# Performance work log

Measured on AMD Instinct MI355X. Metric: run time of the kernel, lower is better.

The kernel has to match this reference:

```python
import jax, jax.numpy as jnp
import numpy as np

NH = 8      # num_heads
AG = 49     # agent_num
PS = 7      # pool_size = sqrt(agent_num)


def _pool_mat(in_size, out_size):
    # torch AdaptiveAvgPool2d bin boundaries: start=floor(i*n/o), end=ceil((i+1)*n/o)
    P = np.zeros((out_size, in_size), dtype=np.float32)
    for i in range(out_size):
        s = (i * in_size) // out_size
        e = -((-(i + 1) * in_size) // out_size)
        P[i, s:e] = 1.0 / (e - s)
    return jnp.asarray(P)


def setup_inputs() -> dict:
    key = jax.random.key(0)
    ks = jax.random.split(key, 16)
    b, n, dim, ic, cc = 32, 1024, 512, 512, 256
    s = 0.02
    d = {}
    d['x'] = jax.random.normal(ks[0], (b, n, dim), jnp.float32)
    d['context'] = jax.random.normal(ks[1], (b, n, cc), jnp.float32)
    d['Wq'] = jax.random.normal(ks[2], (dim, ic), jnp.float32) * s
    d['Wkv'] = jax.random.normal(ks[3], (dim, 2 * ic), jnp.float32) * s
    d['conv_w'] = jax.random.normal(ks[4], (ic, ic + cc, 3, 3), jnp.float32) * s
    d['conv_b'] = jnp.zeros((ic,), jnp.float32)
    d['dwc_w'] = jax.random.normal(ks[5], (ic, 1, 3, 3), jnp.float32) * s
    d['dwc_b'] = jnp.zeros((ic,), jnp.float32)
    d['proj_w'] = jax.random.normal(ks[6], (ic, dim), jnp.float32) * s
    d['proj_b'] = jnp.zeros((dim,), jnp.float32)
    d['an_bias'] = jax.random.normal(ks[7], (NH, AG, 7, 7), jnp.float32) * s
    d['na_bias'] = jax.random.normal(ks[8], (NH, AG, 7, 7), jnp.float32) * s
    d['ah_bias'] = jax.random.normal(ks[9], (1, NH, AG, 32, 1), jnp.float32) * s
    d['aw_bias'] = jax.random.normal(ks[10], (1, NH, AG, 1, 32), jnp.float32) * s
    d['ha_bias'] = jax.random.normal(ks[11], (1, NH, 32, 1, AG), jnp.float32) * s
    d['wa_bias'] = jax.random.normal(ks[12], (1, NH, 1, 32, AG), jnp.float32) * s
    d['H'] = 32; d['W'] = 32; d['c_H'] = 32; d['c_W'] = 32
    return d


def reference(x, context, Wq, Wkv, conv_w, conv_b, dwc_w, dwc_b, proj_w, proj_b,
              an_bias, na_bias, ah_bias, aw_bias, ha_bias, wa_bias, H, W, c_H, c_W):
    b, n, _ = x.shape
    ic = Wq.shape[1]
    cc = context.shape[-1]
    nh, ag = NH, AG
    hd = ic // nh
    scale = hd ** -0.5

    q = x @ Wq                                    # (b, n, ic)
    kv = (x @ Wkv).reshape(b, n, 2, ic)
    k, v = kv[:, :, 0], kv[:, :, 1]

    # adaptive avg pool of q and context down to (PS, PS) agent grid
    Ph, Pw = _pool_mat(H, PS), _pool_mat(W, PS)
    Pch, Pcw = _pool_mat(c_H, PS), _pool_mat(c_W, PS)
    q_img = q.reshape(b, H, W, ic).transpose(0, 3, 1, 2)            # (b, ic, H, W)
    pool_x = jnp.einsum('ph,bchw,qw->bcpq', Ph, q_img, Pw).reshape(b, ic, ag).transpose(0, 2, 1)
    c_img = context.reshape(b, c_H, c_W, cc).transpose(0, 3, 1, 2)  # (b, cc, cH, cW)
    pool_c = jnp.einsum('ph,bchw,qw->bcpq', Pch, c_img, Pcw).reshape(b, cc, ag).transpose(0, 2, 1)

    # NOTE: raw row-major reshape (b, 49, ic+cc) -> (b, ic+cc, 7, 7), exactly as in torch source
    agent = jnp.concatenate([pool_x, pool_c], axis=2).reshape(b, ic + cc, PS, PS)
    agent = jax.lax.conv_general_dilated(agent, conv_w, (1, 1), ((1, 1), (1, 1))) + conv_b[None, :, None, None]
    agent = agent.reshape(b, ic, ag)
    # NOTE: raw reshape (b, ic, 49) -> (b, 49, nh, hd), as in torch source
    a_t = agent.reshape(b, ag, nh, hd).transpose(0, 2, 1, 3)        # (b, nh, ag, hd)

    qh = q.reshape(b, n, nh, hd).transpose(0, 2, 1, 3)
    kh = k.reshape(b, n, nh, hd).transpose(0, 2, 1, 3)
    vh = v.reshape(b, n, nh, hd).transpose(0, 2, 1, 3)

    # agent -> token attention with interpolated + separable relative bias
    pb1 = jax.image.resize(an_bias, (nh, ag, H, W), 'bilinear').reshape(1, nh, ag, n)
    pb2 = (ah_bias + aw_bias).reshape(1, nh, ag, n)
    agent_attn = jax.nn.softmax(jnp.einsum('bhad,bhnd->bhan', a_t * scale, kh) + pb1 + pb2, axis=-1)
    agent_v = jnp.einsum('bhan,bhnd->bhad', agent_attn, vh)         # (b, nh, ag, hd)

    # token -> agent attention
    ab1 = jax.image.resize(na_bias, (nh, ag, H, W), 'bilinear').reshape(1, nh, ag, n).transpose(0, 1, 3, 2)
    ab2 = (ha_bias + wa_bias).reshape(1, nh, n, ag)
    q_attn = jax.nn.softmax(jnp.einsum('bhnd,bhad->bhna', qh * scale, a_t) + ab1 + ab2, axis=-1)
    out = jnp.einsum('bhna,bhad->bhnd', q_attn, agent_v).transpose(0, 2, 1, 3).reshape(b, n, ic)

    # depthwise conv positional encoding on v
    v_img = v.reshape(b, H, W, ic).transpose(0, 3, 1, 2)
    dwc = jax.lax.conv_general_dilated(v_img, dwc_w, (1, 1), ((1, 1), (1, 1)),
                                       feature_group_count=ic) + dwc_b[None, :, None, None]
    out = out + dwc.transpose(0, 2, 3, 1).reshape(b, n, ic)
    return out @ proj_w + proj_b
```

## Files before the change

kernel.cpp:

```cpp
#include <hip/hip_runtime.h>
#include <stdint.h>


typedef __attribute__((ext_vector_type(8)))  short          bf16x8;
typedef __attribute__((ext_vector_type(4)))  float          f32x4;
typedef __attribute__((ext_vector_type(4)))  unsigned short u16x4;

__device__ __forceinline__ float bf2f(unsigned short u) {
    union { unsigned int i; float f; } x; x.i = ((unsigned int)u) << 16; return x.f;
}
__device__ __forceinline__ unsigned short f2bf(float f) {
    union { float f; unsigned int i; } x; x.f = f;
    unsigned int i = x.i;
    i += 0x7FFFu + ((i >> 16) & 1u);
    return (unsigned short)(i >> 16);
}

__global__ void cvt_f32_bf16_kernel(const float* __restrict__ src,
                                    unsigned short* __restrict__ dst) {
    const int i = (blockIdx.x * 256 + threadIdx.x) * 4;
    const f32x4 v = *(const f32x4*)(src + i);
    u16x4 o; o[0]=f2bf(v[0]); o[1]=f2bf(v[1]); o[2]=f2bf(v[2]); o[3]=f2bf(v[3]);
    *(u16x4*)(dst + i) = o;
}

__global__ void build_wqkvt_kernel(const float* __restrict__ Wq,
                                   const float* __restrict__ Wkv,
                                   unsigned short* __restrict__ out) {
    const int idx = blockIdx.x * 256 + threadIdx.x;
    if (idx >= 1536*512) return;
    const int nn = idx >> 9, kk = idx & 511;
    float v = (nn < 512) ? Wq[kk*512 + nn] : Wkv[kk*1024 + (nn - 512)];
    out[idx] = f2bf(v);
}

__global__ void build_projwt_kernel(const float* __restrict__ W,
                                    unsigned short* __restrict__ out) {
    const int idx = blockIdx.x * 256 + threadIdx.x;
    if (idx >= 512*512) return;
    const int nn = idx >> 9, kk = idx & 511;
    out[idx] = f2bf(W[kk*512 + nn]);
}

__device__ __forceinline__ void bilin_coef(int i, int& i0, int& i1, float& f) {
    float pos = (i + 0.5f) * (7.0f / 32.0f) - 0.5f;
    float fl = floorf(pos);
    i0 = (int)fl; f = pos - fl;
    if (i0 < 0)       { i0 = 0; i1 = 0; f = 0.f; }
    else if (i0 >= 6) { i0 = 6; i1 = 6; f = 0.f; }
    else              { i1 = i0 + 1; }
}
__device__ __forceinline__ float bilin7(const float* __restrict__ s, int y, int x) {
    int y0,y1,x0,x1; float fy,fx;
    bilin_coef(y, y0, y1, fy); bilin_coef(x, x0, x1, fx);
    return (1.f-fy)*((1.f-fx)*s[y0*7+x0] + fx*s[y0*7+x1])
         +      fy *((1.f-fx)*s[y1*7+x0] + fx*s[y1*7+x1]);
}

__global__ void bias_prep_kernel(const float* __restrict__ an, const float* __restrict__ na,
                                 const float* __restrict__ ah, const float* __restrict__ aw,
                                 const float* __restrict__ ha, const float* __restrict__ wa,
                                 float* __restrict__ bias1, float* __restrict__ bias2) {
    int idx = blockIdx.x * 256 + threadIdx.x;
    if (idx < 8*49*1024) {
        const int nn = idx & 1023;
        const int a  = (idx >> 10) % 49;
        const int h  = idx / (49*1024);
        const int y = nn >> 5, x = nn & 31;
        float v = bilin7(an + (h*49 + a)*49, y, x)
                + ah[(h*49 + a)*32 + y] + aw[(h*49 + a)*32 + x];
        bias1[idx] = v;
    } else {
        idx -= 8*49*1024;
        if (idx >= 8*1024*49) return;
        const int a  = idx % 49;
        const int nn = (idx / 49) & 1023;
        const int h  = idx / (49*1024);
        const int y = nn >> 5, x = nn & 31;
        float v = bilin7(na + (h*49 + a)*49, y, x)
                + ha[h*1568 + y*49 + a] + wa[h*1568 + x*49 + a];
        bias2[idx] = v;
    }
}

__global__ void pool_kernel(const unsigned short* __restrict__ qkv,
                            const float* __restrict__ context,
                            float* __restrict__ pooled) {
    const int idx = blockIdx.x * 256 + threadIdx.x;
    if (idx >= 32*49*768) return;
    const int c = idx % 768;
    const int a = (idx / 768) % 49;
    const int b = idx / (768*49);
    const int p = a / 7, q = a % 7;
    const int ys = p*32/7, ye = (p*32 + 38)/7;
    const int xs = q*32/7, xe = (q*32 + 38)/7;
    float s = 0.f;
    if (c < 512) {
        for (int y = ys; y < ye; ++y)
            for (int x = xs; x < xe; ++x)
                s += bf2f(qkv[(size_t)(b*1024 + y*32 + x)*1536 + c]);
    } else {
        for (int y = ys; y < ye; ++y)
            for (int x = xs; x < xe; ++x)
                s += context[(size_t)(b*1024 + y*32 + x)*256 + (c - 512)];
    }
    pooled[idx] = s / (float)((ye - ys)*(xe - xs));
}

__global__ void im2col_kernel(const float* __restrict__ pooled,
                              unsigned short* __restrict__ i2c) {
    const int idx = blockIdx.x * 256 + threadIdx.x;
    if (idx >= 1568*6912) return;
    const int kk = idx % 6912;
    const int m  = idx / 6912;
    const int b = m / 49, spq = m % 49;
    const int p = spq / 7, q = spq % 7;
    const int ci = kk / 9, r = kk % 9;
    const int dy = r / 3, dx = r % 3;
    const int yy = p + dy - 1, xx = q + dx - 1;
    float v = 0.f;
    if (yy >= 0 && yy < 7 && xx >= 0 && xx < 7)
        v = pooled[b*37632 + ci*49 + yy*7 + xx];
    i2c[idx] = f2bf(v);
}

template <int MODE>
__launch_bounds__(256)
__global__ void gemm_nt(const unsigned short* __restrict__ A,
                        const unsigned short* __restrict__ Bt,
                        void* __restrict__ C,
                        const float* __restrict__ bias,
                        int K, int ldc, int kspan) {
    __shared__ __align__(16) unsigned char smem_raw[32768];
    unsigned short* As = (unsigned short*)smem_raw;
    unsigned short* Bs = (unsigned short*)(smem_raw + 16384);

    const int gx  = gridDim.x;
    const int gxy = gridDim.x * gridDim.y;
    const int nwg = gxy * gridDim.z;
    const int L   = (blockIdx.z * gridDim.y + blockIdx.y) * gx + blockIdx.x;
    const int qq  = nwg >> 3, rr = nwg & 7;
    const int xcd = L & 7,   ii = L >> 3;
    const int W   = (xcd < rr ? xcd * (qq + 1) : rr * (qq + 1) + (xcd - rr) * qq) + ii;
    const int bz  = W / gxy;
    const int rem = W - bz * gxy;
    const int by  = rem / gx;
    const int bx  = rem - by * gx;

    const int tid  = threadIdx.x;
    const int wid  = tid >> 6;
    const int lane = tid & 63;
    const int m0 = by * 128;
    const int n0 = bx * 128;
    const int wm = (wid >> 1) * 64;
    const int wn = (wid & 1) * 64;
    const int lrow = lane & 15;
    const int quad = lane >> 4;
    const int srow = lane >> 3;
    const int scol = ((lane & 7) ^ srow) * 8;

    f32x4 acc[4][4];
#pragma unroll
    for (int i = 0; i < 4; ++i)
#pragma unroll
        for (int j = 0; j < 4; ++j) acc[i][j] = (f32x4){0.f,0.f,0.f,0.f};

    const int kz0 = bz * kspan;
    const int kz1 = min(K, kz0 + kspan);
    for (int k0 = kz0; k0 < kz1; k0 += 64) {
        __syncthreads();
#pragma unroll
        for (int i = 0; i < 4; ++i) {
            const int chunk = wid*4 + i;
            const int row = chunk*8 + srow;
            __builtin_amdgcn_global_load_lds(
                (const __attribute__((address_space(1))) void*)(A + (size_t)(m0 + row)*K + k0 + scol),
                (__attribute__((address_space(3))) void*)(As + chunk*512), 16, 0, 0);
            __builtin_amdgcn_global_load_lds(
                (const __attribute__((address_space(1))) void*)(Bt + (size_t)(n0 + row)*K + k0 + scol),
                (__attribute__((address_space(3))) void*)(Bs + chunk*512), 16, 0, 0);
        }
        __syncthreads();
#pragma unroll
        for (int kk = 0; kk < 2; ++kk) {
            bf16x8 af[4], bfr[4];
#pragma unroll
            for (int mt = 0; mt < 4; ++mt) {
                const int row = wm + mt*16 + lrow;
                const int u = (kk*4 + quad) ^ (row & 7);
                af[mt] = *(const bf16x8*)(As + row*64 + u*8);
            }
#pragma unroll
            for (int nt = 0; nt < 4; ++nt) {
                const int row = wn + nt*16 + lrow;
                const int u = (kk*4 + quad) ^ (row & 7);
                bfr[nt] = *(const bf16x8*)(Bs + row*64 + u*8);
            }
#pragma unroll
            for (int mt = 0; mt < 4; ++mt)
#pragma unroll
                for (int nt = 0; nt < 4; ++nt)
                    acc[mt][nt] = __builtin_amdgcn_mfma_f32_16x16x32_bf16(
                        af[mt], bfr[nt], acc[mt][nt], 0, 0, 0);
        }
    }

    __syncthreads();
    {
        float* Cf = (float*)smem_raw;
#pragma unroll
        for (int half = 0; half < 2; ++half) {
            if ((wid >> 1) == half) {
#pragma unroll
                for (int mt = 0; mt < 4; ++mt)
#pragma unroll
                    for (int nt = 0; nt < 4; ++nt)
#pragma unroll
                        for (int r = 0; r < 4; ++r) {
                            const int mr = mt*16 + quad*4 + r;
                            const int n  = wn + nt*16 + lrow;
                            Cf[mr*128 + (n ^ ((mr & 7) << 2))] = acc[mt][nt][r];
                        }
            }
            __syncthreads();
#pragma unroll
            for (int it = 0; it < 8; ++it) {
                const int idx = it*256 + tid;
                const int row = idx >> 5, c4 = idx & 31;
                const int m = m0 + half*64 + row;
                f32x4 v = *(const f32x4*)(Cf + row*128 + ((c4*4) ^ ((row & 7) << 2)));
                if (MODE == 0) {
                    const f32x4 bb = *(const f32x4*)(bias + n0 + c4*4);
                    v[0]+=bb[0]; v[1]+=bb[1]; v[2]+=bb[2]; v[3]+=bb[3];
                    *(f32x4*)((float*)C + (size_t)m*ldc + n0 + c4*4) = v;
                } else {
                    if (m < 1568)
                        *(f32x4*)((float*)C + ((size_t)bz*1568 + m)*512 + n0 + c4*4) = v;
                }
            }
            __syncthreads();
        }
    }
}

#define STAGE_A(DST, T, Q) do {                                                             \
    _Pragma("unroll")                                                                       \
    for (int l_ = 0; l_ < 2; ++l_) {                                                        \
        const int rb_ = l_*128 + (Q)*64 + wid*8;                                            \
        __builtin_amdgcn_global_load_lds(                                                   \
            (const __attribute__((address_space(1))) void*)                                 \
                (Ag + (size_t)(m0 + rb_ + lr8)*K + (T)*64 + scl),                           \
            (__attribute__((address_space(3))) void*)((DST) + rb_*64), 16, 0, 0);           \
    }                                                                                       \
} while (0)

#define STAGE_B(DST, T, NH) do {                                                            \
    _Pragma("unroll")                                                                       \
    for (int l_ = 0; l_ < 2; ++l_) {                                                        \
        const int w8_ = wid*8;                                                              \
        const int rb_ = l_*128 + ((w8_ >> 5) << 6) + (NH)*32 + (w8_ & 31);                  \
        __builtin_amdgcn_global_load_lds(                                                   \
            (const __attribute__((address_space(1))) void*)                                 \
                (Btg + (size_t)(n0 + rb_ + lr8)*K + (T)*64 + scl),                          \
            (__attribute__((address_space(3))) void*)((DST) + rb_*64), 16, 0, 0);           \
    }                                                                                       \
} while (0)

#define LOAD_A(MH, SRC) do {                                                                \
    _Pragma("unroll")                                                                       \
    for (int m4_ = 0; m4_ < 4; ++m4_)                                                       \
    _Pragma("unroll")                                                                       \
    for (int kk_ = 0; kk_ < 2; ++kk_)                                                       \
        aF[m4_][kk_] = *(const bf16x8*)                                                     \
            ((SRC) + (wr*128 + ((MH)*4 + m4_)*16 + l15)*64                                  \
                   + (((kk_*4 + quad) ^ sw7) * 8));                                         \
} while (0)

#define LOAD_B(NH, DSTF, SRC) do {                                                          \
    _Pragma("unroll")                                                                       \
    for (int n2_ = 0; n2_ < 2; ++n2_)                                                       \
    _Pragma("unroll")                                                                       \
    for (int kk_ = 0; kk_ < 2; ++kk_)                                                       \
        DSTF[n2_][kk_] = *(const bf16x8*)                                                   \
            ((SRC) + (wc*64 + ((NH)*2 + n2_)*16 + l15)*64                                   \
                   + (((kk_*4 + quad) ^ sw7) * 8));                                         \
} while (0)

#define MFMA_PHASE(MH, NH, BF) do {                                                         \
    __builtin_amdgcn_s_barrier();                                                           \
    asm volatile("s_waitcnt lgkmcnt(0)");                                                   \
    __builtin_amdgcn_sched_barrier(0);                                                      \
    __builtin_amdgcn_s_setprio(1);                                                          \
    _Pragma("unroll")                                                                       \
    for (int kk_ = 0; kk_ < 2; ++kk_)                                                       \
    _Pragma("unroll")                                                                       \
    for (int m4_ = 0; m4_ < 4; ++m4_)                                                       \
    _Pragma("unroll")                                                                       \
    for (int n2_ = 0; n2_ < 2; ++n2_)                                                       \
        acc[(MH)*4 + m4_][(NH)*2 + n2_] = __builtin_amdgcn_mfma_f32_16x16x32_bf16(          \
            aF[m4_][kk_], BF[n2_][kk_], acc[(MH)*4 + m4_][(NH)*2 + n2_], 0, 0, 0);          \
    __builtin_amdgcn_s_setprio(0);                                                          \
    __builtin_amdgcn_sched_barrier(0);                                                      \
} while (0)

template <int MODE>
__launch_bounds__(512, 1)
__global__ void gemm_nt8(const unsigned short* __restrict__ Ag,
                         const unsigned short* __restrict__ Btg,
                         void* __restrict__ C,
                         const float* __restrict__ bias,
                         int K, int ldc) {
    __shared__ unsigned short AsB[2][16384];
    __shared__ unsigned short BsB[2][16384];

    const int gx  = gridDim.x;
    const int nwg = gx * gridDim.y;
    const int L   = blockIdx.y * gx + blockIdx.x;
    const int qq  = nwg >> 3, rr = nwg & 7;
    const int xcd = L & 7,   ii = L >> 3;
    const int W   = (xcd < rr ? xcd * (qq + 1) : rr * (qq + 1) + (xcd - rr) * qq) + ii;
    const int bx  = W % gx, by = W / gx;
    const int m0  = by * 256, n0 = bx * 256;

    const int tid  = threadIdx.x;
    const int wid  = tid >> 6, lane = tid & 63;
    const int wr   = wid >> 2, wc = wid & 3;
    const int l15  = lane & 15, quad = lane >> 4;
    const int lr8  = lane >> 3;
    const int scl  = ((lane & 7) ^ lr8) * 8;
    const int sw7  = l15 & 7;
    const int KT   = K >> 6;

    unsigned short *Acur = &AsB[0][0], *Anxt = &AsB[1][0];
    unsigned short *Bcur = &BsB[0][0], *Bnxt = &BsB[1][0];

    f32x4 acc[8][4];
#pragma unroll
    for (int i = 0; i < 8; ++i)
#pragma unroll
        for (int j = 0; j < 4; ++j) acc[i][j] = (f32x4){0.f,0.f,0.f,0.f};

    bf16x8 aF[4][2], bF0[2][2], bF1[2][2];

    STAGE_A(Acur, 0, 0); STAGE_B(Bcur, 0, 1); STAGE_A(Acur, 0, 1); STAGE_B(Bcur, 0, 0);
    STAGE_A(Anxt, 1, 0); STAGE_B(Bnxt, 1, 1); STAGE_A(Anxt, 1, 1);
    asm volatile("s_waitcnt vmcnt(6)");
    __builtin_amdgcn_s_barrier();

    for (int t = 0; t < KT; ++t) {
        LOAD_B(0, bF0, Bcur);
        LOAD_A(0, Acur);
        if (t + 1 < KT) STAGE_B(Bnxt, t + 1, 0);
        MFMA_PHASE(0, 0, bF0);
        __builtin_amdgcn_s_barrier();

        LOAD_B(1, bF1, Bcur);
        if (t + 2 < KT) STAGE_A(Acur, t + 2, 0);
        MFMA_PHASE(0, 1, bF1);
        __builtin_amdgcn_s_barrier();

        LOAD_A(1, Acur);
        if (t + 2 < KT) STAGE_B(Bcur, t + 2, 1);
        MFMA_PHASE(1, 1, bF1);
        __builtin_amdgcn_s_barrier();

        LOAD_B(0, bF0, Bcur);
        if (t + 2 < KT) STAGE_A(Acur, t + 2, 1);
        MFMA_PHASE(1, 0, bF0);
        if (t + 2 < KT) asm volatile("s_waitcnt vmcnt(6)");
        else            asm volatile("s_waitcnt vmcnt(0)");
        __builtin_amdgcn_s_barrier();

        unsigned short* tmp;
        tmp = Acur; Acur = Anxt; Anxt = tmp;
        tmp = Bcur; Bcur = Bnxt; Bnxt = tmp;
    }

    if (MODE == 1) {
#pragma unroll
        for (int mt = 0; mt < 8; ++mt)
#pragma unroll
            for (int nt = 0; nt < 4; ++nt)
#pragma unroll
                for (int r = 0; r < 4; ++r) {
                    const int m = m0 + wr*128 + mt*16 + quad*4 + r;
                    const int n = n0 + wc*64  + nt*16 + l15;
                    ((unsigned short*)C)[(size_t)m*ldc + n] = f2bf(acc[mt][nt][r]);
                }
    } else {
        float bv[4];
#pragma unroll
        for (int nt = 0; nt < 4; ++nt) bv[nt] = bias[n0 + wc*64 + nt*16 + l15];
#pragma unroll
        for (int mt = 0; mt < 8; ++mt)
#pragma unroll
            for (int nt = 0; nt < 4; ++nt)
#pragma unroll
                for (int r = 0; r < 4; ++r) {
                    const int m = m0 + wr*128 + mt*16 + quad*4 + r;
                    const int n = n0 + wc*64  + nt*16 + l15;
                    ((float*)C)[(size_t)m*ldc + n] = acc[mt][nt][r] + bv[nt];
                }
    }
}

#undef STAGE_A
#undef STAGE_B
#undef LOAD_A
#undef LOAD_B
#undef MFMA_PHASE

__global__ void convred_kernel(const float* __restrict__ part,
                               const float* __restrict__ bias,
                               unsigned short* __restrict__ at_bf) {
    const int idx = blockIdx.x * 256 + threadIdx.x;
    if (idx >= 1568*128) return;
    const int m  = idx >> 7;
    const int n4 = (idx & 127) * 4;
    f32x4 s = *(const f32x4*)&part[(size_t)m*512 + n4];
#pragma unroll
    for (int kz = 1; kz < 9; ++kz) {
        const f32x4 p = *(const f32x4*)&part[((size_t)kz*1568 + m)*512 + n4];
        s[0]+=p[0]; s[1]+=p[1]; s[2]+=p[2]; s[3]+=p[3];
    }
    u16x4 o;
    o[0] = f2bf(s[0] + bias[n4+0]);
    o[1] = f2bf(s[1] + bias[n4+1]);
    o[2] = f2bf(s[2] + bias[n4+2]);
    o[3] = f2bf(s[3] + bias[n4+3]);
    *(u16x4*)&at_bf[(size_t)m*512 + n4] = o;
}

__launch_bounds__(256)
__global__ void agent_attn_mfma_kernel(const unsigned short* __restrict__ qkv,
                                       const unsigned short* __restrict__ at_bf,
                                       const float* __restrict__ bias1,
                                       float* __restrict__ pn,
                                       float* __restrict__ pd) {
    const int bh = blockIdx.x;
    const int b = bh >> 3, h = bh & 7;
    const int sl = blockIdx.y;
    __shared__ unsigned short at_s[64*72];
    __shared__ __align__(16) unsigned char smem[4*64*72*2 + 4*64*64*2];
    unsigned short* P_s = (unsigned short*)smem;
    unsigned short* V_s = (unsigned short*)(smem + 36864);
    float* red  = (float*)smem;
    float* dred = (float*)(smem + 65536);
    const int tid  = threadIdx.x;
    const int wid  = tid >> 6, lane = tid & 63;
    const int l15  = lane & 15, quad = lane >> 4;
    const int j0   = sl*256 + wid*64;

    for (int i = tid; i < 64*72; i += 256) at_s[i] = 0;
    __syncthreads();
    for (int i = tid; i < 49*16; i += 256) {
        const int a = i >> 4, dq = (i & 15) * 4;
        *(u16x4*)&at_s[a*72 + dq] = *(const u16x4*)&at_bf[(size_t)(b*49 + a)*512 + h*64 + dq];
    }
#pragma unroll
    for (int i = 0; i < 8; ++i) {
        __builtin_amdgcn_global_load_lds(
            (const __attribute__((address_space(1))) void*)
                (qkv + (size_t)(b*1024 + j0 + i*8 + (lane>>3))*1536 + 1024 + h*64 + (lane&7)*8),
            (__attribute__((address_space(3))) void*)(V_s + wid*4096 + i*512), 16, 0, 0);
    }
    bf16x8 kfr[4][2];
#pragma unroll
    for (int nt = 0; nt < 4; ++nt)
#pragma unroll
        for (int kf = 0; kf < 2; ++kf)
            kfr[nt][kf] = *(const bf16x8*)
                (qkv + (size_t)(b*1024 + j0 + nt*16 + l15)*1536 + 512 + h*64 + kf*32 + quad*8);
    __syncthreads();

    bf16x8 af[4][2];
#pragma unroll
    for (int mt = 0; mt < 4; ++mt)
#pragma unroll
        for (int kf = 0; kf < 2; ++kf)
            af[mt][kf] = *(const bf16x8*)(at_s + (mt*16 + l15)*72 + kf*32 + quad*8);

    f32x4 acc[4][4];
#pragma unroll
    for (int i = 0; i < 4; ++i)
#pragma unroll
        for (int j = 0; j < 4; ++j) acc[i][j] = (f32x4){0.f,0.f,0.f,0.f};
#pragma unroll
    for (int kf = 0; kf < 2; ++kf)
#pragma unroll
        for (int mt = 0; mt < 4; ++mt)
#pragma unroll
            for (int nt = 0; nt < 4; ++nt)
                acc[mt][nt] = __builtin_amdgcn_mfma_f32_16x16x32_bf16(
                    af[mt][kf], kfr[nt][kf], acc[mt][nt], 0, 0, 0);

    float denp[4][4];
#pragma unroll
    for (int mt = 0; mt < 4; ++mt)
#pragma unroll
        for (int r = 0; r < 4; ++r) denp[mt][r] = 0.f;
#pragma unroll
    for (int mt = 0; mt < 4; ++mt) {
#pragma unroll
        for (int nt = 0; nt < 4; ++nt) {
#pragma unroll
            for (int r = 0; r < 4; ++r) {
                const int a  = mt*16 + quad*4 + r;
                const int ab = (a < 49) ? a : 48;
                const int jj = j0 + nt*16 + l15;
                const float e = __expf(fmaf(0.125f, acc[mt][nt][r],
                                            bias1[(h*49 + ab)*1024 + jj]));
                denp[mt][r] += e;
                P_s[wid*4608 + a*72 + nt*16 + l15] = f2bf(e);
            }
        }
    }
    __syncthreads();

    f32x4 out[4][4];
#pragma unroll
    for (int i = 0; i < 4; ++i)
#pragma unroll
        for (int j = 0; j < 4; ++j) out[i][j] = (f32x4){0.f,0.f,0.f,0.f};
#pragma unroll
    for (int kf = 0; kf < 2; ++kf) {
        bf16x8 va[4];
#pragma unroll
        for (int mt = 0; mt < 4; ++mt) {
            union { bf16x8 v; unsigned short s[8]; } u;
#pragma unroll
            for (int t = 0; t < 8; ++t)
                u.s[t] = V_s[wid*4096 + (kf*32 + quad*8 + t)*64 + mt*16 + l15];
            va[mt] = u.v;
        }
#pragma unroll
        for (int nt = 0; nt < 4; ++nt) {
            const bf16x8 pb = *(const bf16x8*)(P_s + wid*4608 + (nt*16 + l15)*72 + kf*32 + quad*8);
#pragma unroll
            for (int mt = 0; mt < 4; ++mt)
                out[mt][nt] = __builtin_amdgcn_mfma_f32_16x16x32_bf16(
                    va[mt], pb, out[mt][nt], 0, 0, 0);
        }
    }

#pragma unroll
    for (int mt = 0; mt < 4; ++mt) {
#pragma unroll
        for (int r = 0; r < 4; ++r) {
            float v = denp[mt][r];
            v += __shfl_xor(v, 1);
            v += __shfl_xor(v, 2);
            v += __shfl_xor(v, 4);
            v += __shfl_xor(v, 8);
            denp[mt][r] = v;
        }
    }

    __syncthreads();
#pragma unroll
    for (int nt = 0; nt < 4; ++nt) {
        const int a = nt*16 + l15;
#pragma unroll
        for (int mt = 0; mt < 4; ++mt)
            *(f32x4*)&red[wid*4096 + a*64 + mt*16 + quad*4] = out[mt][nt];
    }
    if (l15 == 0) {
#pragma unroll
        for (int mt = 0; mt < 4; ++mt)
#pragma unroll
            for (int r = 0; r < 4; ++r)
                dred[wid*64 + mt*16 + quad*4 + r] = denp[mt][r];
    }
    __syncthreads();
    for (int i = tid; i < 4096; i += 256) {
        const float s = red[i] + red[4096 + i] + red[8192 + i] + red[12288 + i];
        pn[((size_t)bh*4 + sl)*4096 + i] = s;
    }
    if (tid < 64) {
        const float s = dred[tid] + dred[64 + tid] + dred[128 + tid] + dred[192 + tid];
        pd[((size_t)bh*4 + sl)*64 + tid] = s;
    }
}

__global__ void agent_combine_kernel(const float* __restrict__ pn,
                                     const float* __restrict__ pd,
                                     unsigned short* __restrict__ avT) {
    const int idx = blockIdx.x * 256 + threadIdx.x;
    if (idx >= 256*4096) return;
    const int bh = idx >> 12;
    const int i  = idx & 4095;
    const int a = i >> 6, d = i & 63;
    float num = 0.f, den = 0.f;
#pragma unroll
    for (int s = 0; s < 4; ++s) {
        num += pn[(((size_t)bh*4 + s)*64 + a)*64 + d];
        den += pd[((size_t)bh*4 + s)*64 + a];
    }
    avT[(size_t)bh*4096 + d*64 + a] = (a < 49) ? f2bf(num / den) : (unsigned short)0;
}

__launch_bounds__(256)
__global__ void qattn_mfma_kernel(const unsigned short* __restrict__ qkv,
                                  const unsigned short* __restrict__ at_bf,
                                  const unsigned short* __restrict__ avT,
                                  const float* __restrict__ bias2,
                                  const float* __restrict__ dwc_w,
                                  const float* __restrict__ dwc_b,
                                  unsigned short* __restrict__ out_pre) {
    const int bh = blockIdx.x;
    const int b = bh >> 3, h = bh & 7;
    const int tq = blockIdx.y;
    __shared__ __align__(16) unsigned char smem[69632];
    unsigned short* P_s = (unsigned short*)smem;
    float* out_s = (float*)smem;
    __shared__ float dwcw_s[64*9];
    __shared__ float dwcb_s[64];
    const int tid = threadIdx.x;
    const int wid = tid >> 6, lane = tid & 63;
    const int l15 = lane & 15, quad = lane >> 4;
    const int j0  = tq*256 + wid*64;

    for (int i = tid; i < 64*9; i += 256) dwcw_s[i] = dwc_w[h*576 + i];
    if (tid < 64) dwcb_s[tid] = dwc_b[h*64 + tid];

    bf16x8 qa[4][2];
#pragma unroll
    for (int mt = 0; mt < 4; ++mt)
#pragma unroll
        for (int kf = 0; kf < 2; ++kf)
            qa[mt][kf] = *(const bf16x8*)
                (qkv + (size_t)(b*1024 + j0 + mt*16 + l15)*1536 + h*64 + kf*32 + quad*8);
    bf16x8 ab[4][2];
#pragma unroll
    for (int nt = 0; nt < 4; ++nt) {
        const int a  = nt*16 + l15;
        const int ar = (a < 49) ? a : 48;
#pragma unroll
        for (int kf = 0; kf < 2; ++kf)
            ab[nt][kf] = *(const bf16x8*)
                (at_bf + (size_t)(b*49 + ar)*512 + h*64 + kf*32 + quad*8);
    }

    f32x4 e[4][4];
#pragma unroll
    for (int i = 0; i < 4; ++i)
#pragma unroll
        for (int j = 0; j < 4; ++j) e[i][j] = (f32x4){0.f,0.f,0.f,0.f};
#pragma unroll
    for (int kf = 0; kf < 2; ++kf)
#pragma unroll
        for (int mt = 0; mt < 4; ++mt)
#pragma unroll
            for (int nt = 0; nt < 4; ++nt)
                e[mt][nt] = __builtin_amdgcn_mfma_f32_16x16x32_bf16(
                    qa[mt][kf], ab[nt][kf], e[mt][nt], 0, 0, 0);

    float denp[4][4];
#pragma unroll
    for (int mt = 0; mt < 4; ++mt)
#pragma unroll
        for (int r = 0; r < 4; ++r) denp[mt][r] = 0.f;
#pragma unroll
    for (int mt = 0; mt < 4; ++mt) {
#pragma unroll
        for (int nt = 0; nt < 4; ++nt) {
            const int a = nt*16 + l15;
#pragma unroll
            for (int r = 0; r < 4; ++r) {
                if (a < 49) {
                    const int jj = j0 + mt*16 + quad*4 + r;
                    const float v = __expf(fmaf(0.125f, e[mt][nt][r],
                                                bias2[((size_t)h*1024 + jj)*49 + a]));
                    e[mt][nt][r] = v;
                    denp[mt][r] += v;
                } else {
                    e[mt][nt][r] = 0.f;
                }
            }
        }
    }
#pragma unroll
    for (int mt = 0; mt < 4; ++mt) {
#pragma unroll
        for (int r = 0; r < 4; ++r) {
            float v = denp[mt][r];
            v += __shfl_xor(v, 1);
            v += __shfl_xor(v, 2);
            v += __shfl_xor(v, 4);
            v += __shfl_xor(v, 8);
            denp[mt][r] = 1.0f / v;
        }
    }
#pragma unroll
    for (int mt = 0; mt < 4; ++mt)
#pragma unroll
        for (int nt = 0; nt < 4; ++nt)
#pragma unroll
            for (int r = 0; r < 4; ++r)
                P_s[wid*4608 + (mt*16 + quad*4 + r)*72 + nt*16 + l15] =
                    f2bf(e[mt][nt][r] * denp[mt][r]);

    bf16x8 bv[4][2];
#pragma unroll
    for (int nt = 0; nt < 4; ++nt)
#pragma unroll
        for (int kf = 0; kf < 2; ++kf)
            bv[nt][kf] = *(const bf16x8*)
                (avT + (size_t)bh*4096 + (nt*16 + l15)*64 + kf*32 + quad*8);
    f32x4 out[4][4];
#pragma unroll
    for (int i = 0; i < 4; ++i)
#pragma unroll
        for (int j = 0; j < 4; ++j) out[i][j] = (f32x4){0.f,0.f,0.f,0.f};
#pragma unroll
    for (int kf = 0; kf < 2; ++kf) {
        bf16x8 pa[4];
#pragma unroll
        for (int mt = 0; mt < 4; ++mt)
            pa[mt] = *(const bf16x8*)(P_s + wid*4608 + (mt*16 + l15)*72 + kf*32 + quad*8);
#pragma unroll
        for (int nt = 0; nt < 4; ++nt)
#pragma unroll
            for (int mt = 0; mt < 4; ++mt)
                out[mt][nt] = __builtin_amdgcn_mfma_f32_16x16x32_bf16(
                    pa[mt], bv[nt][kf], out[mt][nt], 0, 0, 0);
    }

    __syncthreads();
#pragma unroll
    for (int mt = 0; mt < 4; ++mt)
#pragma unroll
        for (int nt = 0; nt < 4; ++nt)
#pragma unroll
            for (int r = 0; r < 4; ++r)
                out_s[(wid*64 + mt*16 + quad*4 + r)*68 + nt*16 + l15] = out[mt][nt][r];
    __syncthreads();

    const int tt = tid >> 2;
    const int p  = tid & 3;
    const int d0 = p*16;
    for (int it = 0; it < 4; ++it) {
        const int tl = it*64 + tt;
        const int jj = tq*256 + tl;
        float o[16];
#pragma unroll
        for (int i = 0; i < 16; ++i) o[i] = out_s[tl*68 + d0 + i] + dwcb_s[d0 + i];
        const int y = jj >> 5, x = jj & 31;
#pragma unroll
        for (int dy = 0; dy < 3; ++dy) {
            const int yy = y + dy - 1;
            if (yy < 0 || yy > 31) continue;
#pragma unroll
            for (int dx = 0; dx < 3; ++dx) {
                const int xx = x + dx - 1;
                if (xx < 0 || xx > 31) continue;
                const unsigned short* vp =
                    qkv + (size_t)(b*1024 + yy*32 + xx)*1536 + 1024 + h*64 + d0;
#pragma unroll
                for (int i4 = 0; i4 < 4; ++i4) {
                    const u16x4 v4 = *(const u16x4*)(vp + i4*4);
#pragma unroll
                    for (int i = 0; i < 4; ++i)
                        o[i4*4+i] = fmaf(dwcw_s[(d0 + i4*4 + i)*9 + dy*3 + dx],
                                         bf2f(v4[i]), o[i4*4+i]);
                }
            }
        }
        unsigned short* op = out_pre + (size_t)(b*1024 + jj)*512 + h*64 + d0;
#pragma unroll
        for (int i4 = 0; i4 < 4; ++i4) {
            u16x4 w;
            w[0]=f2bf(o[i4*4+0]); w[1]=f2bf(o[i4*4+1]);
            w[2]=f2bf(o[i4*4+2]); w[3]=f2bf(o[i4*4+3]);
            *(u16x4*)(op + i4*4) = w;
        }
    }
}

extern "C" void kernel_launch(void* const* d_in, const int* in_sizes, int n_in,
                              void* d_out, int out_size, void* d_ws, size_t ws_size,
                              hipStream_t stream) {
    (void)in_sizes; (void)n_in; (void)out_size; (void)ws_size;
    const float* x       = (const float*)d_in[0];
    const float* context = (const float*)d_in[1];
    const float* Wq      = (const float*)d_in[2];
    const float* Wkv     = (const float*)d_in[3];
    const float* conv_w  = (const float*)d_in[4];
    const float* conv_b  = (const float*)d_in[5];
    const float* dwc_w   = (const float*)d_in[6];
    const float* dwc_b   = (const float*)d_in[7];
    const float* proj_w  = (const float*)d_in[8];
    const float* proj_b  = (const float*)d_in[9];
    const float* an_bias = (const float*)d_in[10];
    const float* na_bias = (const float*)d_in[11];
    const float* ah_bias = (const float*)d_in[12];
    const float* aw_bias = (const float*)d_in[13];
    const float* ha_bias = (const float*)d_in[14];
    const float* wa_bias = (const float*)d_in[15];

    char* ws = (char*)d_ws;
    size_t off = 0;
    auto alloc = [&](size_t bytes) -> char* {
        char* p = ws + off; off += (bytes + 255) & ~(size_t)255; return p;
    };
    unsigned short* xb     = (unsigned short*)alloc((size_t)16777216 * 2);
    unsigned short* qkv    = (unsigned short*)alloc((size_t)50331648 * 2);
    unsigned short* wqkvt  = (unsigned short*)alloc((size_t)786432  * 2);
    unsigned short* projwt = (unsigned short*)alloc((size_t)262144  * 2);
    unsigned short* convwb = (unsigned short*)alloc((size_t)3538944 * 2);
    float*          pooled = (float*)alloc((size_t)1204224 * 4);
    unsigned short* i2c    = (unsigned short*)alloc((size_t)1664*6912*2);
    unsigned short* at_bf  = (unsigned short*)alloc((size_t)1568*512*2);
    float*          bias1  = (float*)alloc((size_t)401408 * 4);
    float*          bias2  = (float*)alloc((size_t)401408 * 4);
    unsigned short* avT    = (unsigned short*)alloc((size_t)256*4096*2);
    float*          part_conv = (float*)xb;
    float*          pn        = (float*)i2c;
    float*          pd        = pn + (size_t)256*4*64*64;
    unsigned short* outpre    = xb;

    cvt_f32_bf16_kernel<<<16384, 256, 0, stream>>>(x, xb);
    cvt_f32_bf16_kernel<<<3456, 256, 0, stream>>>(conv_w, convwb);
    build_wqkvt_kernel<<<3072, 256, 0, stream>>>(Wq, Wkv, wqkvt);
    build_projwt_kernel<<<1024, 256, 0, stream>>>(proj_w, projwt);
    bias_prep_kernel<<<3136, 256, 0, stream>>>(an_bias, na_bias, ah_bias, aw_bias,
                                               ha_bias, wa_bias, bias1, bias2);
    gemm_nt8<1><<<dim3(6, 128), 512, 0, stream>>>(xb, wqkvt, qkv, nullptr, 512, 1536);
    pool_kernel<<<4704, 256, 0, stream>>>(qkv, context, pooled);
    im2col_kernel<<<42336, 256, 0, stream>>>(pooled, i2c);
    gemm_nt<3><<<dim3(4, 13, 9), 256, 0, stream>>>(i2c, convwb, part_conv, nullptr, 6912, 512, 768);
    convred_kernel<<<784, 256, 0, stream>>>(part_conv, conv_b, at_bf);
    agent_attn_mfma_kernel<<<dim3(256, 4), 256, 0, stream>>>(qkv, at_bf, bias1, pn, pd);
    agent_combine_kernel<<<4096, 256, 0, stream>>>(pn, pd, avT);
    qattn_mfma_kernel<<<dim3(256, 4), 256, 0, stream>>>(qkv, at_bf, avT, bias2,
                                                        dwc_w, dwc_b, outpre);
    gemm_nt8<0><<<dim3(2, 128), 512, 0, stream>>>(outpre, projwt, d_out, proj_b, 512, 512);
}
```

Before: 477.7 us.

## Fuse x bf16 conversion into QKV GEMM and merge small prep kernels

Removes the separate pass that converts x from fp32 to bf16 and replaces the QKV GEMM with a new kernel. The new kernel stages fp32 A tiles into LDS and converts them to bf16 in registers before the MFMA. It also merges the weight-transpose and bias-prep kernels into one launch to cut launch overhead. The cost is twice the LDS footprint and traffic for the A tile, a single-buffered main loop, and scalar bf16 output stores in place of the tuned 8-wave GEMM.

```diff
diff --git a/kernel.cpp b/kernel.cpp
--- a/kernel.cpp
+++ b/kernel.cpp
@@ -22,24 +22,6 @@
     const f32x4 v = *(const f32x4*)(src + i);
     u16x4 o; o[0]=f2bf(v[0]); o[1]=f2bf(v[1]); o[2]=f2bf(v[2]); o[3]=f2bf(v[3]);
     *(u16x4*)(dst + i) = o;
-}
-
-__global__ void build_wqkvt_kernel(const float* __restrict__ Wq,
-                                   const float* __restrict__ Wkv,
-                                   unsigned short* __restrict__ out) {
-    const int idx = blockIdx.x * 256 + threadIdx.x;
-    if (idx >= 1536*512) return;
-    const int nn = idx >> 9, kk = idx & 511;
-    float v = (nn < 512) ? Wq[kk*512 + nn] : Wkv[kk*1024 + (nn - 512)];
-    out[idx] = f2bf(v);
-}
-
-__global__ void build_projwt_kernel(const float* __restrict__ W,
-                                    unsigned short* __restrict__ out) {
-    const int idx = blockIdx.x * 256 + threadIdx.x;
-    if (idx >= 512*512) return;
-    const int nn = idx >> 9, kk = idx & 511;
-    out[idx] = f2bf(W[kk*512 + nn]);
 }
 
 __device__ __forceinline__ void bilin_coef(int i, int& i0, int& i1, float& f) {
@@ -57,11 +39,30 @@
          +      fy *((1.f-fx)*s[y1*7+x0] + fx*s[y1*7+x1]);
 }
 
-__global__ void bias_prep_kernel(const float* __restrict__ an, const float* __restrict__ na,
-                                 const float* __restrict__ ah, const float* __restrict__ aw,
-                                 const float* __restrict__ ha, const float* __restrict__ wa,
-                                 float* __restrict__ bias1, float* __restrict__ bias2) {
+__global__ void prep_small_kernel(const float* __restrict__ Wq,
+                                  const float* __restrict__ Wkv,
+                                  const float* __restrict__ Wproj,
+                                  const float* __restrict__ an, const float* __restrict__ na,
+                                  const float* __restrict__ ah, const float* __restrict__ aw,
+                                  const float* __restrict__ ha, const float* __restrict__ wa,
+                                  unsigned short* __restrict__ wqkvt,
+                                  unsigned short* __restrict__ projwt,
+                                  float* __restrict__ bias1,
+                                  float* __restrict__ bias2) {
     int idx = blockIdx.x * 256 + threadIdx.x;
+    if (idx < 786432) {
+        const int nn = idx >> 9, kk = idx & 511;
+        float v = (nn < 512) ? Wq[kk*512 + nn] : Wkv[kk*1024 + (nn - 512)];
+        wqkvt[idx] = f2bf(v);
+        return;
+    }
+    idx -= 786432;
+    if (idx < 262144) {
+        const int nn = idx >> 9, kk = idx & 511;
+        projwt[idx] = f2bf(Wproj[kk*512 + nn]);
+        return;
+    }
+    idx -= 262144;
     if (idx < 8*49*1024) {
         const int nn = idx & 1023;
         const int a  = (idx >> 10) % 49;
@@ -243,6 +244,104 @@
     }
 }
 
+__launch_bounds__(256)
+__global__ void gemm_qkv_f32a(const float* __restrict__ Ax,
+                              const unsigned short* __restrict__ Bt,
+                              unsigned short* __restrict__ C) {
+    __shared__ __align__(16) float          Asf[128*64];
+    __shared__ __align__(16) unsigned short Bs[128*64];
+
+    const int gx  = 12;
+    const int L   = blockIdx.y * gx + blockIdx.x;
+    const int qq  = 3072 >> 3;
+    const int xcd = L & 7, ii = L >> 3;
+    const int W   = xcd * qq + ii;
+    const int bx  = W % gx, by = W / gx;
+    const int m0  = by * 128, n0 = bx * 128;
+
+    const int tid  = threadIdx.x;
+    const int wid  = tid >> 6;
+    const int lane = tid & 63;
+    const int wm = (wid >> 1) * 64;
+    const int wn = (wid & 1) * 64;
+    const int lrow = lane & 15;
+    const int quad = lane >> 4;
+    const int srow = lane >> 3;
+    const int scol = ((lane & 7) ^ srow) * 8;
+    const int arow = lane >> 4;
+    const int c4e  = (lane & 15) ^ arow;
+    const int c4o  = (lane & 15) ^ (4 | arow);
+
+    f32x4 acc[4][4];
+#pragma unroll
+    for (int i = 0; i < 4; ++i)
+#pragma unroll
+        for (int j = 0; j < 4; ++j) acc[i][j] = (f32x4){0.f,0.f,0.f,0.f};
+
+    for (int k0 = 0; k0 < 512; k0 += 64) {
+        __syncthreads();
+#pragma unroll
+        for (int i = 0; i < 4; ++i) {
+            const int chunk = wid*4 + i;
+            const int row = chunk*8 + srow;
+            __builtin_amdgcn_global_load_lds(
+                (const __attribute__((address_space(1))) void*)(Bt + (size_t)(n0 + row)*512 + k0 + scol),
+                (__attribute__((address_space(3))) void*)(Bs + chunk*512), 16, 0, 0);
+        }
+#pragma unroll
+        for (int i = 0; i < 8; ++i) {
+            const int chunk = wid*8 + i;
+            const int c4g = (chunk & 1) ? c4o : c4e;
+            __builtin_amdgcn_global_load_lds(
+                (const __attribute__((address_space(1))) void*)
+                    (Ax + (size_t)(m0 + chunk*4 + arow)*512 + k0 + c4g*4),
+                (__attribute__((address_space(3))) void*)(Asf + chunk*256), 16, 0, 0);
+        }
+        __syncthreads();
+#pragma unroll
+        for (int kk = 0; kk < 2; ++kk) {
+            bf16x8 af[4], bfr[4];
+#pragma unroll
+            for (int mt = 0; mt < 4; ++mt) {
+                const int row = wm + mt*16 + lrow;
+                const int r7  = lrow & 7;
+                const int bu  = kk*8 + quad*2;
+                const f32x4 lo = *(const f32x4*)(Asf + row*64 + (((bu    ) ^ r7) << 2));
+                const f32x4 hi = *(const f32x4*)(Asf + row*64 + (((bu + 1) ^ r7) << 2));
+                union { unsigned int d[4]; bf16x8 v; } u;
+                asm("v_cvt_pk_bf16_f32 %0, %1, %2" : "=v"(u.d[0]) : "v"(lo[0]), "v"(lo[1]));
+                asm("v_cvt_pk_bf16_f32 %0, %1, %2" : "=v"(u.d[1]) : "v"(lo[2]), "v"(lo[3]));
+                asm("v_cvt_pk_bf16_f32 %0, %1, %2" : "=v"(u.d[2]) : "v"(hi[0]), "v"(hi[1]));
+                asm("v_cvt_pk_bf16_f32 %0, %1, %2" : "=v"(u.d[3]) : "v"(hi[2]), "v"(hi[3]));
+                af[mt] = u.v;
+            }
+#pragma unroll
+            for (int nt = 0; nt < 4; ++nt) {
+                const int row = wn + nt*16 + lrow;
+                const int ub = (kk*4 + quad) ^ (row & 7);
+                bfr[nt] = *(const bf16x8*)(Bs + row*64 + ub*8);
+            }
+#pragma unroll
+            for (int mt = 0; mt < 4; ++mt)
+#pragma unroll
+                for (int nt = 0; nt < 4; ++nt)
+                    acc[mt][nt] = __builtin_amdgcn_mfma_f32_16x16x32_bf16(
+                        af[mt], bfr[nt], acc[mt][nt], 0, 0, 0);
+        }
+    }
+
+#pragma unroll
+    for (int mt = 0; mt < 4; ++mt)
+#pragma unroll
+        for (int nt = 0; nt < 4; ++nt)
+#pragma unroll
+            for (int r = 0; r < 4; ++r) {
+                const int m = m0 + wm + mt*16 + quad*4 + r;
+                const int n = n0 + wn + nt*16 + lrow;
+                C[(size_t)m*1536 + n] = f2bf(acc[mt][nt][r]);
+            }
+}
+
 #define STAGE_A(DST, T, Q) do {                                                             \
     _Pragma("unroll")                                                                       \
     for (int l_ = 0; l_ < 2; ++l_) {                                                        \
@@ -819,13 +918,12 @@
     float*          pd        = pn + (size_t)256*4*64*64;
     unsigned short* outpre    = xb;
 
-    cvt_f32_bf16_kernel<<<16384, 256, 0, stream>>>(x, xb);
     cvt_f32_bf16_kernel<<<3456, 256, 0, stream>>>(conv_w, convwb);
-    build_wqkvt_kernel<<<3072, 256, 0, stream>>>(Wq, Wkv, wqkvt);
-    build_projwt_kernel<<<1024, 256, 0, stream>>>(proj_w, projwt);
-    bias_prep_kernel<<<3136, 256, 0, stream>>>(an_bias, na_bias, ah_bias, aw_bias,
-                                               ha_bias, wa_bias, bias1, bias2);
-    gemm_nt8<1><<<dim3(6, 128), 512, 0, stream>>>(xb, wqkvt, qkv, nullptr, 512, 1536);
+    prep_small_kernel<<<7232, 256, 0, stream>>>(Wq, Wkv, proj_w,
+                                                an_bias, na_bias, ah_bias, aw_bias,
+                                                ha_bias, wa_bias,
+                                                wqkvt, projwt, bias1, bias2);
+    gemm_qkv_f32a<<<dim3(12, 256), 256, 0, stream>>>(x, wqkvt, qkv);
     pool_kernel<<<4704, 256, 0, stream>>>(qkv, context, pooled);
     im2col_kernel<<<42336, 256, 0, stream>>>(pooled, i2c);
     gemm_nt<3><<<dim3(4, 13, 9), 256, 0, stream>>>(i2c, convwb, part_conv, nullptr, 6912, 512, 768);
```

Measured after the change: 479.3 us. Within noise of the previous version (+0.3%).
